# Optimization experiments

Hardware: AMD Instinct MI355X
Metric: run time of the kernel (lower is better)

The kernel has to match this reference:

```python
import jax, jax.numpy as jnp
import numpy as np

N = 16384       # nodes (hits in one event)
IN_DIM = 9      # input features per hit
HID = 128       # hidden_dim
PROP = 64       # propagate_dimensions; 2*PROP == HID so all gravnet layers share shapes
SPACE = 4       # learned space dimensions
K = 40          # neighbors (includes self, matching torch_cluster.knn)
L = 4           # num_gravnet_layers
OUT_DIM = 4


def _lin(key, fan_in, fan_out):
    # torch nn.Linear default init: U(-1/sqrt(fan_in), 1/sqrt(fan_in))
    k1, k2 = jax.random.split(key)
    lim = 1.0 / np.sqrt(fan_in)
    W = jax.random.uniform(k1, (fan_in, fan_out), minval=-lim, maxval=lim, dtype=jnp.float32)
    b = jax.random.uniform(k2, (fan_out,), minval=-lim, maxval=lim, dtype=jnp.float32)
    return W, b


def _stack_lin(key, fan_in, fan_out, n):
    Ws, bs = [], []
    for i in range(n):
        W, b = _lin(jax.random.fold_in(key, i), fan_in, fan_out)
        Ws.append(W); bs.append(b)
    return jnp.stack(Ws), jnp.stack(bs)


def setup_inputs() -> dict:
    key = jax.random.key(0)
    ks = jax.random.split(key, 16)
    inp = {}
    inp['x'] = jax.random.normal(ks[0], (N, IN_DIM), dtype=jnp.float32)
    inp['fc1_W'], inp['fc1_b'] = _lin(ks[1], IN_DIM, HID)
    inp['fc2_W'], inp['fc2_b'] = _lin(ks[2], HID, HID)
    # GravNetConv params (in_channels = HID = 2*PROP for every layer)
    inp['gs_W'], inp['gs_b'] = _stack_lin(ks[3], HID, SPACE, L)          # lin_s
    inp['gh_W'], inp['gh_b'] = _stack_lin(ks[4], HID, PROP, L)           # lin_h
    inp['go_W'], inp['go_b'] = _stack_lin(ks[5], HID + 2 * PROP, 2 * PROP, L)  # lin_out
    # dense_after_gravnet: Linear(2P->HID), Linear(HID->HID), Linear(HID->2P)
    inp['d1_W'], inp['d1_b'] = _stack_lin(ks[6], 2 * PROP, HID, L)
    inp['d2_W'], inp['d2_b'] = _stack_lin(ks[7], HID, HID, L)
    inp['d3_W'], inp['d3_b'] = _stack_lin(ks[8], HID, 2 * PROP, L)
    inp['fc3_W'], inp['fc3_b'] = _lin(ks[9], 2 * PROP, HID)
    inp['fc4_W'], inp['fc4_b'] = _lin(ks[10], HID, OUT_DIM)
    return inp


def _gravnet_layer(x, sW, sb, hW, hb, oW, ob):
    # PyG GravNetConv: s = lin_s(x), h = lin_h(x); kNN in s-space (self included);
    # edge weight exp(-10*d^2); message h_j*w; aggr = [mean, max]; out = lin_out([x, aggr]).
    s = x @ sW + sb                               # [N, SPACE]
    h = x @ hW + hb                               # [N, PROP]
    s2 = jnp.sum(s * s, axis=1)
    d2 = s2[:, None] + s2[None, :] - 2.0 * (s @ s.T)   # [N, N] squared distances
    neg_d2, idx = jax.lax.top_k(-d2, K)           # k nearest (self is its own nearest)
    w = jnp.exp(10.0 * jnp.minimum(neg_d2, 0.0))  # exp(-10*d2), clamped d2 >= 0
    msg = h[idx] * w[..., None]                   # [N, K, PROP] gather + weight
    agg = jnp.concatenate([msg.mean(axis=1), msg.max(axis=1)], axis=-1)  # [N, 2P]
    return jnp.concatenate([x, agg], axis=-1) @ oW + ob


def reference(x, fc1_W, fc1_b, fc2_W, fc2_b, gs_W, gs_b, gh_W, gh_b, go_W, go_b,
              d1_W, d1_b, d2_W, d2_b, d3_W, d3_b, fc3_W, fc3_b, fc4_W, fc4_b):
    relu = jax.nn.relu
    x = relu(x @ fc1_W + fc1_b)
    x = relu(x @ fc2_W + fc2_b)
    for i in range(L):  # small fixed layer count
        x = _gravnet_layer(x, gs_W[i], gs_b[i], gh_W[i], gh_b[i], go_W[i], go_b[i])
        x = relu(x @ d1_W[i] + d1_b[i])
        x = relu(x @ d2_W[i] + d2_b[i])
        x = relu(x @ d3_W[i] + d3_b[i])
    x = relu(x @ fc3_W + fc3_b)
    return x @ fc4_W + fc4_b
```

## Files before the change

kernel.cpp:

```cpp
#include <hip/hip_runtime.h>
#include <math.h>

#define NPTS     16384
#define KNN_K    40
#define KNN_CAPW 320

typedef unsigned short u16;
typedef __attribute__((ext_vector_type(8))) short bf16x8;
typedef __attribute__((ext_vector_type(4))) float f32x4;

static __device__ __forceinline__ float bf2f(unsigned short h) {
  return __uint_as_float(((unsigned)h) << 16);
}
static __device__ __forceinline__ unsigned short f2bf(float f) {
  unsigned u = __float_as_uint(f);
  unsigned r = (u + 0x7fffu + ((u >> 16) & 1u)) >> 16;
  return (unsigned short)r;
}
static __device__ __forceinline__ float ldf(const float* p) { return *p; }
static __device__ __forceinline__ float ldf(const unsigned short* p) { return bf2f(*p); }

static __device__ __forceinline__ float rfl(float x) {
  return __uint_as_float(__builtin_amdgcn_readfirstlane(__float_as_uint(x)));
}
static __device__ __forceinline__ unsigned mbcnt64(unsigned long long m) {
  return __builtin_amdgcn_mbcnt_hi((unsigned)(m >> 32),
                                   __builtin_amdgcn_mbcnt_lo((unsigned)m, 0u));
}

static __device__ __forceinline__ unsigned encf(float f) {
  unsigned b = __float_as_uint(f);
  return (b & 0x80000000u) ? ~b : (b | 0x80000000u);
}
static __device__ __forceinline__ float decf(unsigned e) {
  unsigned b = (e & 0x80000000u) ? (e ^ 0x80000000u) : ~e;
  return __uint_as_float(b);
}

#define WSPLIT_ELEMS 393216

__global__ __launch_bounds__(256, 8) void wsplit_k(
    const float* __restrict__ fc2W, const float* __restrict__ ghW,
    const float* __restrict__ goW,  const float* __restrict__ d1W,
    const float* __restrict__ d2W,  const float* __restrict__ d3W,
    const float* __restrict__ fc3W, u16* __restrict__ out)
{
  int e = blockIdx.x * 256 + threadIdx.x;
  const float* W; int base, lM;
  if (e < 16384)       { W = fc2W; base = 0;      lM = 7; }
  else if (e < 49152)  { W = ghW;  base = 16384;  lM = 6; }
  else if (e < 180224) { W = goW;  base = 49152;  lM = 7; }
  else if (e < 245760) { W = d1W;  base = 180224; lM = 7; }
  else if (e < 311296) { W = d2W;  base = 245760; lM = 7; }
  else if (e < 376832) { W = d3W;  base = 311296; lM = 7; }
  else                 { W = fc3W; base = 376832; lM = 7; }
  int li = e - base;
  int M = 1 << lM;
  int k = li >> lM, n = li & (M - 1);
  float wv = W[li];
  u16 hi = f2bf(wv);
  u16 lo = f2bf(wv - bf2f(hi));
  int kb = k >> 5, kk = k & 31;
  u16* ob = out + 2 * base + kb * (M << 6);
  ob[n * 32 + kk] = hi;
  ob[(M << 5) + n * 32 + kk] = lo;
}

template<int MCOLS, bool RELU>
__global__ __launch_bounds__(256, 2) void gemm_mfma_k(
    const u16* __restrict__ A1, int lda1,
    const u16* __restrict__ A2, int lda2, int K1,
    const u16* __restrict__ Wsp, const float* __restrict__ bias,
    u16* __restrict__ C, int ldc, int K)
{
  constexpr int CT = MCOLS / 64;
  constexpr int AST = 40;
  __shared__ u16 lds[64 * AST + 2 * MCOLS * AST];
  u16* As = lds;
  u16* Wh = lds + 64 * AST;
  u16* Wl = Wh + MCOLS * AST;

  const int tid = threadIdx.x;
  const int lane = tid & 63;
  const int w = tid >> 6;
  const int row0 = blockIdx.x * 64;

  f32x4 acc[4][CT];
  #pragma unroll
  for (int rt = 0; rt < 4; ++rt)
    #pragma unroll
    for (int ct = 0; ct < CT; ++ct)
      acc[rt][ct] = (f32x4){0.f, 0.f, 0.f, 0.f};

  const int rbase = lane & 15;
  const int koff = (lane >> 4) * 8;

  for (int k0 = 0, kb = 0; k0 < K; k0 += 32, ++kb) {
    __syncthreads();
    {
      int r = tid >> 2, seg = tid & 3;
      int kk = k0 + seg * 8;
      const u16* src = (kk < K1) ? &A1[(size_t)(row0 + r) * lda1 + kk]
                                 : &A2[(size_t)(row0 + r) * lda2 + (kk - K1)];
      *(uint4*)&As[r * AST + seg * 8] = *(const uint4*)src;
    }
    {
      const u16* wsb = Wsp + (size_t)kb * (MCOLS << 6);
      #pragma unroll
      for (int l = tid; l < 2 * MCOLS * 4; l += 256) {
        int r = l >> 2, seg = l & 3;
        *(uint4*)&Wh[r * AST + seg * 8] = *(const uint4*)&wsb[r * 32 + seg * 8];
      }
    }
    __syncthreads();

    bf16x8 a[4];
    #pragma unroll
    for (int rt = 0; rt < 4; ++rt)
      a[rt] = *(const bf16x8*)&As[(rt * 16 + rbase) * AST + koff];
    #pragma unroll
    for (int ct = 0; ct < CT; ++ct) {
      int col = (w * CT + ct) * 16 + rbase;
      bf16x8 bh = *(const bf16x8*)&Wh[col * AST + koff];
      bf16x8 bl = *(const bf16x8*)&Wl[col * AST + koff];
      #pragma unroll
      for (int rt = 0; rt < 4; ++rt) {
        acc[rt][ct] = __builtin_amdgcn_mfma_f32_16x16x32_bf16(a[rt], bh, acc[rt][ct], 0, 0, 0);
        acc[rt][ct] = __builtin_amdgcn_mfma_f32_16x16x32_bf16(a[rt], bl, acc[rt][ct], 0, 0, 0);
      }
    }
  }

  __syncthreads();
  constexpr int CST = MCOLS + 8;
  u16* Ct = lds;
  const int rq = (lane >> 4) * 4;
  #pragma unroll
  for (int ct = 0; ct < CT; ++ct) {
    int col = (w * CT + ct) * 16 + rbase;
    float bv = bias[col];
    #pragma unroll
    for (int rt = 0; rt < 4; ++rt) {
      #pragma unroll
      for (int q = 0; q < 4; ++q) {
        float v = acc[rt][ct][q] + bv;
        if (RELU) v = fmaxf(v, 0.f);
        Ct[(rt * 16 + rq + q) * CST + col] = f2bf(v);
      }
    }
  }
  __syncthreads();
  constexpr int SEGS = MCOLS / 8;
  for (int l = tid; l < 64 * SEGS; l += 256) {
    int r = l / SEGS, sg = l % SEGS;
    *(uint4*)&C[(size_t)(row0 + r) * ldc + sg * 8] = *(const uint4*)&Ct[r * CST + sg * 8];
  }
}

template<int MCOLS, bool RELU>
__global__ __launch_bounds__(256, 2) void gemm_mfma_f32_k(
    const u16* __restrict__ A1, int lda1,
    const u16* __restrict__ A2, int lda2, int K1,
    const float* __restrict__ W, const float* __restrict__ bias,
    u16* __restrict__ C, int ldc, int K)
{
  constexpr int CT = MCOLS / 64;
  constexpr int AST = 40;
  __shared__ u16 lds[64 * AST + 2 * MCOLS * AST];
  u16* As = lds;
  u16* Wh = lds + 64 * AST;
  u16* Wl = Wh + MCOLS * AST;

  const int tid = threadIdx.x;
  const int lane = tid & 63;
  const int w = tid >> 6;
  const int row0 = blockIdx.x * 64;

  f32x4 acc[4][CT];
  #pragma unroll
  for (int rt = 0; rt < 4; ++rt)
    #pragma unroll
    for (int ct = 0; ct < CT; ++ct)
      acc[rt][ct] = (f32x4){0.f, 0.f, 0.f, 0.f};

  const int rbase = lane & 15;
  const int koff = (lane >> 4) * 8;

  for (int k0 = 0; k0 < K; k0 += 32) {
    __syncthreads();
    {
      int r = tid >> 2, seg = tid & 3;
      int kk = k0 + seg * 8;
      const u16* src = (kk < K1) ? &A1[(size_t)(row0 + r) * lda1 + kk]
                                 : &A2[(size_t)(row0 + r) * lda2 + (kk - K1)];
      *(uint4*)&As[r * AST + seg * 8] = *(const uint4*)src;
    }
    for (int l = tid; l < 32 * MCOLS; l += 256) {
      int n = l & (MCOLS - 1), kk = l / MCOLS;
      float wv = W[(size_t)(k0 + kk) * MCOLS + n];
      u16 h = f2bf(wv);
      Wh[n * AST + kk] = h;
      Wl[n * AST + kk] = f2bf(wv - bf2f(h));
    }
    __syncthreads();

    bf16x8 a[4];
    #pragma unroll
    for (int rt = 0; rt < 4; ++rt)
      a[rt] = *(const bf16x8*)&As[(rt * 16 + rbase) * AST + koff];
    #pragma unroll
    for (int ct = 0; ct < CT; ++ct) {
      int col = (w * CT + ct) * 16 + rbase;
      bf16x8 bh = *(const bf16x8*)&Wh[col * AST + koff];
      bf16x8 bl = *(const bf16x8*)&Wl[col * AST + koff];
      #pragma unroll
      for (int rt = 0; rt < 4; ++rt) {
        acc[rt][ct] = __builtin_amdgcn_mfma_f32_16x16x32_bf16(a[rt], bh, acc[rt][ct], 0, 0, 0);
        acc[rt][ct] = __builtin_amdgcn_mfma_f32_16x16x32_bf16(a[rt], bl, acc[rt][ct], 0, 0, 0);
      }
    }
  }

  __syncthreads();
  constexpr int CST = MCOLS + 8;
  u16* Ct = lds;
  const int rq = (lane >> 4) * 4;
  #pragma unroll
  for (int ct = 0; ct < CT; ++ct) {
    int col = (w * CT + ct) * 16 + rbase;
    float bv = bias[col];
    #pragma unroll
    for (int rt = 0; rt < 4; ++rt) {
      #pragma unroll
      for (int q = 0; q < 4; ++q) {
        float v = acc[rt][ct][q] + bv;
        if (RELU) v = fmaxf(v, 0.f);
        Ct[(rt * 16 + rq + q) * CST + col] = f2bf(v);
      }
    }
  }
  __syncthreads();
  constexpr int SEGS = MCOLS / 8;
  for (int l = tid; l < 64 * SEGS; l += 256) {
    int r = l / SEGS, sg = l % SEGS;
    *(uint4*)&C[(size_t)(row0 + r) * ldc + sg * 8] = *(const uint4*)&Ct[r * CST + sg * 8];
  }
}

template<int MCOLS, bool RELU, typename TIN, typename TOUT>
__global__ __launch_bounds__(256, 4) void gemm_k(
    const TIN* __restrict__ A1, int lda1,
    const TIN* __restrict__ A2, int lda2, int K1,
    const float* __restrict__ W, const float* __restrict__ bias,
    TOUT* __restrict__ C, int ldc, int K)
{
  constexpr int TCS = MCOLS / 8;
  constexpr int RPT = (64 * TCS) / 256;
  __shared__ float Asl[64][33];
  __shared__ float Ws[32][MCOLS];
  const int tid = threadIdx.x;
  const int row0 = blockIdx.x * 64;
  const int tc = tid % TCS, tr = tid / TCS;

  float acc[RPT][8];
  #pragma unroll
  for (int p = 0; p < RPT; ++p)
    #pragma unroll
    for (int q = 0; q < 8; ++q) acc[p][q] = 0.f;

  for (int k0 = 0; k0 < K; k0 += 32) {
    __syncthreads();
    for (int l = tid; l < 64 * 32; l += 256) {
      int r = l >> 5, c = l & 31, k = k0 + c;
      float v = 0.f;
      if (k < K) v = (k < K1) ? ldf(&A1[(size_t)(row0 + r) * lda1 + k])
                              : ldf(&A2[(size_t)(row0 + r) * lda2 + (k - K1)]);
      Asl[r][c] = v;
    }
    for (int l = tid; l < 32 * MCOLS; l += 256) {
      int kr = l / MCOLS, c = l % MCOLS, k = k0 + kr;
      Ws[kr][c] = (k < K) ? W[(size_t)k * MCOLS + c] : 0.f;
    }
    __syncthreads();
    #pragma unroll
    for (int kk = 0; kk < 32; ++kk) {
      float a[RPT];
      #pragma unroll
      for (int p = 0; p < RPT; ++p) a[p] = Asl[tr * RPT + p][kk];
      const float4 w0 = *(const float4*)&Ws[kk][tc * 8];
      const float4 w1 = *(const float4*)&Ws[kk][tc * 8 + 4];
      #pragma unroll
      for (int p = 0; p < RPT; ++p) {
        acc[p][0] = fmaf(a[p], w0.x, acc[p][0]);
        acc[p][1] = fmaf(a[p], w0.y, acc[p][1]);
        acc[p][2] = fmaf(a[p], w0.z, acc[p][2]);
        acc[p][3] = fmaf(a[p], w0.w, acc[p][3]);
        acc[p][4] = fmaf(a[p], w1.x, acc[p][4]);
        acc[p][5] = fmaf(a[p], w1.y, acc[p][5]);
        acc[p][6] = fmaf(a[p], w1.z, acc[p][6]);
        acc[p][7] = fmaf(a[p], w1.w, acc[p][7]);
      }
    }
  }

  const float4 b0 = *(const float4*)&bias[tc * 8];
  const float4 b1 = *(const float4*)&bias[tc * 8 + 4];
  #pragma unroll
  for (int p = 0; p < RPT; ++p) {
    int r = row0 + tr * RPT + p;
    float o[8];
    o[0] = acc[p][0] + b0.x; o[1] = acc[p][1] + b0.y;
    o[2] = acc[p][2] + b0.z; o[3] = acc[p][3] + b0.w;
    o[4] = acc[p][4] + b1.x; o[5] = acc[p][5] + b1.y;
    o[6] = acc[p][6] + b1.z; o[7] = acc[p][7] + b1.w;
    if (RELU) {
      #pragma unroll
      for (int q = 0; q < 8; ++q) o[q] = fmaxf(o[q], 0.f);
    }
    if constexpr (sizeof(TOUT) == 2) {
      unsigned p0 = (unsigned)f2bf(o[0]) | ((unsigned)f2bf(o[1]) << 16);
      unsigned p1 = (unsigned)f2bf(o[2]) | ((unsigned)f2bf(o[3]) << 16);
      unsigned p2 = (unsigned)f2bf(o[4]) | ((unsigned)f2bf(o[5]) << 16);
      unsigned p3 = (unsigned)f2bf(o[6]) | ((unsigned)f2bf(o[7]) << 16);
      uint4 pk = make_uint4(p0, p1, p2, p3);
      *(uint4*)&C[(size_t)r * ldc + tc * 8] = pk;
    } else {
      float4 o0, o1;
      o0.x = o[0]; o0.y = o[1]; o0.z = o[2]; o0.w = o[3];
      o1.x = o[4]; o1.y = o[5]; o1.z = o[6]; o1.w = o[7];
      *(float4*)&C[(size_t)r * ldc + tc * 8] = o0;
      *(float4*)&C[(size_t)r * ldc + tc * 8 + 4] = o1;
    }
  }
}

template<bool RELU, bool MM, typename TOUT>
__global__ __launch_bounds__(256, 4) void gemm4_k(
    const u16* __restrict__ A, int lda,
    const float* __restrict__ W, const float* __restrict__ bias,
    TOUT* __restrict__ C, int K, unsigned* mm)
{
  __shared__ float Wsl[128 * 4];
  __shared__ float bl[4];
  const int tid = threadIdx.x;
  for (int l = tid; l < K * 4; l += 256) Wsl[l] = W[l];
  if (tid < 4) bl[tid] = bias[tid];
  __syncthreads();
  const int row = blockIdx.x * 256 + tid;
  const u16* ap = A + (size_t)row * lda;
  float a0 = bl[0], a1 = bl[1], a2 = bl[2], a3 = bl[3];
  for (int k8 = 0; k8 < K; k8 += 8) {
    uint4 pk = *(const uint4*)&ap[k8];
    unsigned uu[4] = {pk.x, pk.y, pk.z, pk.w};
    #pragma unroll
    for (int q = 0; q < 4; ++q) {
      float flo = __uint_as_float(uu[q] << 16);
      float fhi = __uint_as_float(uu[q] & 0xFFFF0000u);
      const float* wr0 = &Wsl[(k8 + 2 * q) * 4];
      a0 = fmaf(flo, wr0[0], a0); a1 = fmaf(flo, wr0[1], a1);
      a2 = fmaf(flo, wr0[2], a2); a3 = fmaf(flo, wr0[3], a3);
      a0 = fmaf(fhi, wr0[4], a0); a1 = fmaf(fhi, wr0[5], a1);
      a2 = fmaf(fhi, wr0[6], a2); a3 = fmaf(fhi, wr0[7], a3);
    }
  }
  if (RELU) {
    a0 = fmaxf(a0, 0.f); a1 = fmaxf(a1, 0.f);
    a2 = fmaxf(a2, 0.f); a3 = fmaxf(a3, 0.f);
  }
  if constexpr (sizeof(TOUT) == 2) {
    C[(size_t)row * 4 + 0] = (TOUT)f2bf(a0);
    C[(size_t)row * 4 + 1] = (TOUT)f2bf(a1);
    C[(size_t)row * 4 + 2] = (TOUT)f2bf(a2);
    C[(size_t)row * 4 + 3] = (TOUT)f2bf(a3);
  } else {
    float4 o; o.x = a0; o.y = a1; o.z = a2; o.w = a3;
    *(float4*)&C[(size_t)row * 4] = o;
  }
  if constexpr (MM) {
    float mn0 = a0, mx0 = a0, mn1 = a1, mx1 = a1;
    float mn2 = a2, mx2 = a2, mn3 = a3, mx3 = a3;
    #pragma unroll
    for (int o = 32; o >= 1; o >>= 1) {
      mn0 = fminf(mn0, __shfl_xor(mn0, o, 64)); mx0 = fmaxf(mx0, __shfl_xor(mx0, o, 64));
      mn1 = fminf(mn1, __shfl_xor(mn1, o, 64)); mx1 = fmaxf(mx1, __shfl_xor(mx1, o, 64));
      mn2 = fminf(mn2, __shfl_xor(mn2, o, 64)); mx2 = fmaxf(mx2, __shfl_xor(mx2, o, 64));
      mn3 = fminf(mn3, __shfl_xor(mn3, o, 64)); mx3 = fmaxf(mx3, __shfl_xor(mx3, o, 64));
    }
    if ((tid & 63) == 0) {
      atomicMin(&mm[0], encf(mn0)); atomicMax(&mm[4], encf(mx0));
      atomicMin(&mm[1], encf(mn1)); atomicMax(&mm[5], encf(mx1));
      atomicMin(&mm[2], encf(mn2)); atomicMax(&mm[6], encf(mx2));
      atomicMin(&mm[3], encf(mn3)); atomicMax(&mm[7], encf(mx3));
    }
  }
}

__global__ void init_mm_k(unsigned* mm) {
  int t = threadIdx.x;
  if (t < 4) { mm[t] = 0xFFFFFFFFu; mm[4 + t] = 0u; }
}

static __device__ __forceinline__ float dimsel(float4 p, int d) {
  return (d == 0) ? p.x : (d == 1) ? p.y : (d == 2) ? p.z : p.w;
}

__global__ __launch_bounds__(1024, 1) void histpref_k(
    const float* __restrict__ S, unsigned* __restrict__ mm,
    unsigned* __restrict__ binoff)
{
  __shared__ unsigned hist[256];
  __shared__ unsigned wsum[4];
  const int tid = threadIdx.x;
  float mn[4], rg[4];
  #pragma unroll
  for (int d = 0; d < 4; ++d) {
    mn[d] = decf(mm[d]);
    rg[d] = decf(mm[4 + d]) - mn[d];
  }
  int a = 0;
  #pragma unroll
  for (int d = 1; d < 4; ++d) if (rg[d] > rg[a]) a = d;
  int b = (a == 0) ? 1 : 0;
  #pragma unroll
  for (int d = 0; d < 4; ++d) if (d != a && rg[d] > rg[b]) b = d;
  float inva = (rg[a] > 0.f) ? (16.f / rg[a]) * 0.999999f : 0.f;
  float invb = (rg[b] > 0.f) ? (16.f / rg[b]) * 0.999999f : 0.f;
  if (tid == 0) {
    mm[8] = (unsigned)a; mm[9] = (unsigned)b;
    mm[10] = __float_as_uint(mn[a]); mm[11] = __float_as_uint(inva);
    mm[12] = __float_as_uint(mn[b]); mm[13] = __float_as_uint(invb);
  }
  if (tid < 256) hist[tid] = 0u;
  __syncthreads();
  for (int i = tid; i < NPTS; i += 1024) {
    float4 p = *(const float4*)&S[(size_t)i * 4];
    int ba = min(15, max(0, (int)((dimsel(p, a) - mn[a]) * inva)));
    int bb = min(15, max(0, (int)((dimsel(p, b) - mn[b]) * invb)));
    atomicAdd(&hist[ba * 16 + bb], 1u);
  }
  __syncthreads();
  unsigned v = 0, x = 0;
  if (tid < 256) {
    int lane = tid & 63;
    v = hist[tid]; x = v;
    #pragma unroll
    for (int o = 1; o < 64; o <<= 1) {
      unsigned t = (unsigned)__shfl_up((int)x, o, 64);
      if (lane >= o) x += t;
    }
    if (lane == 63) wsum[tid >> 6] = x;
  }
  __syncthreads();
  if (tid < 256) {
    unsigned off = 0;
    for (int k = 0; k < (tid >> 6); ++k) off += wsum[k];
    binoff[tid] = off + x - v;
  }
}

__global__ __launch_bounds__(256, 4) void scatter_k(
    const float* __restrict__ S, const unsigned* __restrict__ mm,
    unsigned* __restrict__ binoff,
    float4* __restrict__ SX4, float* __restrict__ SS2, u16* __restrict__ SIDXs)
{
  int a = (int)mm[8], b = (int)mm[9];
  float alo = __uint_as_float(mm[10]), inva = __uint_as_float(mm[11]);
  float blo = __uint_as_float(mm[12]), invb = __uint_as_float(mm[13]);
  int i = blockIdx.x * 256 + threadIdx.x;
  float4 p = *(const float4*)&S[(size_t)i * 4];
  int ba = min(15, max(0, (int)((dimsel(p, a) - alo) * inva)));
  int bb = min(15, max(0, (int)((dimsel(p, b) - blo) * invb)));
  unsigned pos = atomicAdd(&binoff[ba * 16 + bb], 1u);
  SX4[pos] = p;
  SS2[pos] = fmaf(p.x, p.x, fmaf(p.y, p.y, fmaf(p.z, p.z, p.w * p.w)));
  SIDXs[pos] = (u16)i;
}

__global__ __launch_bounds__(512, 4) void gaabb_k(const float4* __restrict__ SX4,
                                                  float* __restrict__ gaabb) {
  int w = threadIdx.x >> 6, lane = threadIdx.x & 63;
  int g = blockIdx.x * 8 + w;
  float4 p = SX4[g * 64 + lane];
  float mnx = p.x, mny = p.y, mnz = p.z, mnw = p.w;
  float mxx = p.x, mxy = p.y, mxz = p.z, mxw = p.w;
  #pragma unroll
  for (int o = 32; o >= 1; o >>= 1) {
    mnx = fminf(mnx, __shfl_xor(mnx, o, 64)); mxx = fmaxf(mxx, __shfl_xor(mxx, o, 64));
    mny = fminf(mny, __shfl_xor(mny, o, 64)); mxy = fmaxf(mxy, __shfl_xor(mxy, o, 64));
    mnz = fminf(mnz, __shfl_xor(mnz, o, 64)); mxz = fmaxf(mxz, __shfl_xor(mxz, o, 64));
    mnw = fminf(mnw, __shfl_xor(mnw, o, 64)); mxw = fmaxf(mxw, __shfl_xor(mxw, o, 64));
  }
  if (lane == 0) {
    float4* gp = (float4*)&gaabb[g * 8];
    gp[0] = make_float4(mnx, mny, mnz, mnw);
    gp[1] = make_float4(mxx, mxy, mxz, mxw);
  }
}

struct CompactRes { int cnt; unsigned thr; };

static __device__ __forceinline__ CompactRes compact_buf(unsigned* bufR, int cnt, int lane) {
  int n = min(cnt, KNN_CAPW);
  int lo = -1, hi = 0x7FFFFFFF, chi = n;
  for (int it = 0; it < 32; ++it) {
    if (chi <= 96) break;
    int mid = lo + ((hi - lo) >> 1);
    int lc = 0;
    for (int base = 0; base < n; base += 64) {
      int i = base + lane;
      bool c = (i < n) && (bufR[i] <= (unsigned)mid);
      lc += (int)__popcll(__ballot(c));
    }
    if (lc >= 40) { hi = mid; chi = lc; } else lo = mid;
  }
  unsigned thr = (unsigned)hi;
  int out = 0;
  for (int base = 0; base < n; base += 64) {
    int i = base + lane;
    unsigned key = (i < n) ? bufR[i] : 0xFFFFFFFFu;
    bool keep = (i < n) && (key <= thr);
    unsigned long long mk = __ballot(keep);
    unsigned pre = mbcnt64(mk);
    if (keep) bufR[out + (int)pre] = key;
    out += (int)__popcll(mk);
  }
  CompactRes r; r.cnt = out; r.thr = thr;
  return r;
}

__global__ __launch_bounds__(256, 4) void knn_k(
    const float4* __restrict__ SX4, const float* __restrict__ SS2,
    const u16* __restrict__ SIDXs, const float* __restrict__ gaabb,
    u16* __restrict__ idx_out, u16* __restrict__ w_out)
{
  __shared__ unsigned buf[4 * 4 * KNN_CAPW];
  __shared__ unsigned scr[4 * 128];
  __shared__ int cnts[16];
  __shared__ unsigned thrend[16];
  __shared__ unsigned short glist[4 * 64];
  __shared__ unsigned long long mws[4];
  __shared__ unsigned thrsh[4];

  const int tid = threadIdx.x;
  const int lane = tid & 63;
  const int w = tid >> 6;
  const int sp0 = blockIdx.x * 4;

  float cx[4], cy[4], cz[4], cw[4], s2r[4], thrF[4];
  int orow[4], cnt[4];
  #pragma unroll
  for (int r = 0; r < 4; ++r) {
    float4 sr = SX4[sp0 + r];
    cx[r] = rfl(-2.f * sr.x); cy[r] = rfl(-2.f * sr.y);
    cz[r] = rfl(-2.f * sr.z); cw[r] = rfl(-2.f * sr.w);
    s2r[r] = rfl(fmaf(sr.x, sr.x, fmaf(sr.y, sr.y, fmaf(sr.z, sr.z, sr.w * sr.w))));
    orow[r] = SIDXs[sp0 + r];
    cnt[r] = 0;
  }
  unsigned* bufw = &buf[w * 4 * KNN_CAPW];
  unsigned* mph = buf;

  {
    int gs = sp0 >> 6;
    int g0 = min(max(gs - 7, 0), 240);
    float m1[4], m2[4];
    #pragma unroll
    for (int r = 0; r < 4; ++r) { m1[r] = 3.0e38f; m2[r] = 3.0e38f; }
    #pragma unroll
    for (int gi = 0; gi < 4; ++gi) {
      int j = (g0 + w * 4 + gi) * 64 + lane;
      float4 p = SX4[j];
      float q = SS2[j];
      #pragma unroll
      for (int r = 0; r < 4; ++r) {
        float d = fmaf(cx[r], p.x, fmaf(cy[r], p.y, fmaf(cz[r], p.z,
                  fmaf(cw[r], p.w, q + s2r[r]))));
        d = fmaxf(d, 0.f);
        bool lt1 = d < m1[r];
        float nm2 = lt1 ? m1[r] : fminf(m2[r], d);
        m1[r] = fminf(m1[r], d);
        m2[r] = nm2;
      }
    }
    #pragma unroll
    for (int r = 0; r < 4; ++r) {
      mph[(r * 8 + w * 2 + 0) * 64 + lane] = __float_as_uint(m1[r]);
      mph[(r * 8 + w * 2 + 1) * 64 + lane] = __float_as_uint(m2[r]);
    }
  }
  __syncthreads();

  {
    unsigned vals[8];
    #pragma unroll
    for (int s = 0; s < 8; ++s) vals[s] = mph[(w * 8 + s) * 64 + lane];
    int lo = -1, hi = 0x7F800000, chi = 512;
    for (int it = 0; it < 32; ++it) {
      if (chi <= 44 || (hi - lo) <= 1) break;
      int mid = lo + ((hi - lo) >> 1);
      int c = 0;
      #pragma unroll
      for (int s = 0; s < 8; ++s)
        c += (int)__popcll(__ballot(vals[s] <= (unsigned)mid));
      if (c >= 40) { hi = mid; chi = c; } else lo = mid;
    }
    if (lane == 0) thrsh[w] = (unsigned)hi;
  }
  __syncthreads();
  #pragma unroll
  for (int r = 0; r < 4; ++r) thrF[r] = __uint_as_float(thrsh[r]);

  {
    int g = w * 64 + lane;
    float4 mn = *(const float4*)&gaabb[g * 8];
    float4 mx = *(const float4*)&gaabb[g * 8 + 4];
    bool want = false;
    #pragma unroll
    for (int r = 0; r < 4; ++r) {
      float px = -0.5f * cx[r], py = -0.5f * cy[r];
      float pz = -0.5f * cz[r], pw = -0.5f * cw[r];
      float dx = fmaxf(fmaxf(mn.x - px, px - mx.x), 0.f);
      float dy = fmaxf(fmaxf(mn.y - py, py - mx.y), 0.f);
      float dz = fmaxf(fmaxf(mn.z - pz, pz - mx.z), 0.f);
      float dw = fmaxf(fmaxf(mn.w - pw, pw - mx.w), 0.f);
      float md = fmaf(dx, dx, fmaf(dy, dy, fmaf(dz, dz, dw * dw)));
      want |= (md <= thrF[r]);
    }
    unsigned long long bal = __ballot(want);
    if (lane == 0) mws[w] = bal;
  }
  __syncthreads();

  int ng = 0;
  {
    int ordbase = 0;
    #pragma unroll
    for (int pgi = 0; pgi < 4; ++pgi) {
      unsigned long long m = mws[pgi];
      bool want = (m >> lane) & 1ull;
      int ord = ordbase + (int)mbcnt64(m);
      if (want && ((ord & 3) == w))
        glist[w * 64 + (ord >> 2)] = (unsigned short)(pgi * 64 + lane);
      ordbase += (int)__popcll(m);
    }
    ng = (ordbase + 3 - w) >> 2;
  }

  if (ng > 0) {
    int j = (int)glist[w * 64] * 64 + lane;
    float4 p = SX4[j];
    float q = SS2[j];
    unsigned sv = (unsigned)j;
    for (int i = 0; i < ng; ++i) {
      float4 pn = p; float qn = q; unsigned svn = sv;
      if (i + 1 < ng) {
        int j2 = (int)glist[w * 64 + i + 1] * 64 + lane;
        pn = SX4[j2]; qn = SS2[j2]; svn = (unsigned)j2;
      }
      #pragma unroll
      for (int r = 0; r < 4; ++r) {
        float d = fmaf(cx[r], p.x, fmaf(cy[r], p.y, fmaf(cz[r], p.z,
                  fmaf(cw[r], p.w, q + s2r[r]))));
        bool k = d <= thrF[r];
        unsigned long long mk = __ballot(k);
        if (mk) {
          int pos = cnt[r] + (int)mbcnt64(mk);
          if (k) bufw[r * KNN_CAPW + pos] =
              (__float_as_uint(fmaxf(d, 0.f)) & 0xFFFFC000u) | sv;
          cnt[r] += (int)__popcll(mk);
          if (cnt[r] >= KNN_CAPW - 64) {
            CompactRes cr = compact_buf(&bufw[r * KNN_CAPW], cnt[r], lane);
            cnt[r] = cr.cnt;
            thrF[r] = __uint_as_float((cr.thr & 0xFFFFC000u) | 0x3FFFu);
          }
        }
      }
      p = pn; q = qn; sv = svn;
    }
  }

  if (lane == 0) {
    #pragma unroll
    for (int r = 0; r < 4; ++r) {
      cnts[w * 4 + r] = cnt[r];
      thrend[w * 4 + r] = (__float_as_uint(thrF[r]) & 0xFFFFC000u) | 0x3FFFu;
    }
  }
  __syncthreads();

  {
    const int rr = w;
    const unsigned* seg[4];
    int c[4], off[5];
    off[0] = 0;
    #pragma unroll
    for (int s = 0; s < 4; ++s) {
      seg[s] = &buf[(s * 4 + rr) * KNN_CAPW];
      c[s] = cnts[s * 4 + rr];
      off[s + 1] = off[s] + c[s];
    }
    int mt = off[4];
    unsigned* S = &scr[rr * 128];

    if (mt > 128) {
      unsigned hi0 = min(min(thrend[0 * 4 + rr], thrend[1 * 4 + rr]),
                         min(thrend[2 * 4 + rr], thrend[3 * 4 + rr]));
      int lc = 0;
      #pragma unroll
      for (int s = 0; s < 4; ++s)
        for (int base = 0; base < c[s]; base += 64) {
          int i = base + lane;
          bool cc = (i < c[s]) && (seg[s][i] <= hi0);
          lc += (int)__popcll(__ballot(cc));
        }
      unsigned thrm = hi0;
      if (lc > 128) {
        int lo = -1, hi = (int)hi0, chi = lc;
        for (int it = 0; it < 32; ++it) {
          if (chi <= 96) break;
          int mid = lo + ((hi - lo) >> 1);
          int lc2 = 0;
          #pragma unroll
          for (int s = 0; s < 4; ++s)
            for (int base = 0; base < c[s]; base += 64) {
              int i = base + lane;
              bool cc = (i < c[s]) && (seg[s][i] <= (unsigned)mid);
              lc2 += (int)__popcll(__ballot(cc));
            }
          if (lc2 >= 40) { hi = mid; chi = lc2; } else lo = mid;
        }
        thrm = (unsigned)hi;
      }
      int out = 0;
      #pragma unroll
      for (int s = 0; s < 4; ++s)
        for (int base = 0; base < c[s]; base += 64) {
          int i = base + lane;
          unsigned key = (i < c[s]) ? seg[s][i] : 0xFFFFFFFFu;
          bool keep = (i < c[s]) && (key <= thrm);
          unsigned long long mk = __ballot(keep);
          int pos = out + (int)mbcnt64(mk);
          if (keep && pos < 128) S[pos] = key;
          out += (int)__popcll(mk);
        }
      mt = min(out, 128);
    } else {
      #pragma unroll
      for (int s = 0; s < 4; ++s)
        for (int base = 0; base < c[s]; base += 64) {
          int i = base + lane;
          if (i < c[s]) S[off[s] + i] = seg[s][i];
        }
    }

    const float fx = cx[rr], fy = cy[rr], fz = cz[rr], fw = cw[rr];
    const float s2i = s2r[rr];
    const int row = orow[rr];

    unsigned long long e0 = ~0ull, e1 = ~0ull;
    {
      int sl0 = lane * 2, sl1 = lane * 2 + 1;
      if (sl0 < mt) {
        unsigned key = S[sl0];
        unsigned sj = key & 0x3FFFu;
        float4 p = SX4[sj];
        float qj = fmaf(p.x, p.x, fmaf(p.y, p.y, fmaf(p.z, p.z, p.w * p.w)));
        float d = fmaf(fx, p.x, fmaf(fy, p.y, fmaf(fz, p.z, fmaf(fw, p.w, qj + s2i))));
        unsigned oi = (unsigned)SIDXs[sj];
        e0 = (((unsigned long long)__float_as_uint(fmaxf(d, 0.f))) << 32) | oi;
      }
      if (sl1 < mt) {
        unsigned key = S[sl1];
        unsigned sj = key & 0x3FFFu;
        float4 p = SX4[sj];
        float qj = fmaf(p.x, p.x, fmaf(p.y, p.y, fmaf(p.z, p.z, p.w * p.w)));
        float d = fmaf(fx, p.x, fmaf(fy, p.y, fmaf(fz, p.z, fmaf(fw, p.w, qj + s2i))));
        unsigned oi = (unsigned)SIDXs[sj];
        e1 = (((unsigned long long)__float_as_uint(fmaxf(d, 0.f))) << 32) | oi;
      }
    }

    #pragma unroll
    for (int k = 2; k <= 128; k <<= 1) {
      #pragma unroll
      for (int jj = k >> 1; jj >= 1; jj >>= 1) {
        bool up = (((lane * 2) & k) == 0);
        if (jj == 1) {
          unsigned long long a = (e0 < e1) ? e0 : e1;
          unsigned long long b = (e0 < e1) ? e1 : e0;
          e0 = up ? a : b; e1 = up ? b : a;
        } else {
          int lj = jj >> 1;
          bool lower = ((lane & lj) == 0);
          bool tm = (up == lower);
          unsigned long long o0 = __shfl_xor(e0, lj, 64);
          e0 = tm ? ((e0 < o0) ? e0 : o0) : ((e0 > o0) ? e0 : o0);
          unsigned long long o1 = __shfl_xor(e1, lj, 64);
          e1 = tm ? ((e1 < o1) ? e1 : o1) : ((e1 > o1) ? e1 : o1);
        }
      }
    }

    const int ob = row * KNN_K;
    if (lane < 20) {
      int v0 = lane * 2;
      idx_out[ob + v0] = (unsigned short)(e0 & 0xFFFFu);
      w_out[ob + v0] = f2bf(__expf(-10.f * __uint_as_float((unsigned)(e0 >> 32))));
      int v1 = v0 + 1;
      idx_out[ob + v1] = (unsigned short)(e1 & 0xFFFFu);
      w_out[ob + v1] = f2bf(__expf(-10.f * __uint_as_float((unsigned)(e1 >> 32))));
    }
  }
}

__global__ __launch_bounds__(256, 4) void agg_k(
    const unsigned short* __restrict__ h, const unsigned short* __restrict__ idxb,
    const unsigned short* __restrict__ wb, unsigned short* __restrict__ Aout)
{
  const int row = blockIdx.x * 4 + (threadIdx.x >> 6);
  const int lane = threadIdx.x & 63;
  const int base = row * KNN_K;
  float mean = 0.f, mx = -INFINITY;
  #pragma unroll 4
  for (int k = 0; k < KNN_K; ++k) {
    int j = idxb[base + k];
    float wv = bf2f(wb[base + k]);
    float m = bf2f(h[(size_t)j * 64 + lane]) * wv;
    mean += m;
    mx = fmaxf(mx, m);
  }
  Aout[(size_t)row * 128 + lane] = f2bf(mean * (1.f / 40.f));
  Aout[(size_t)row * 128 + 64 + lane] = f2bf(mx);
}

extern "C" void kernel_launch(void* const* d_in, const int* in_sizes, int n_in,
                              void* d_out, int out_size, void* d_ws, size_t ws_size,
                              hipStream_t stream)
{
  const float* x    = (const float*)d_in[0];
  const float* fc1W = (const float*)d_in[1];  const float* fc1b = (const float*)d_in[2];
  const float* fc2W = (const float*)d_in[3];  const float* fc2b = (const float*)d_in[4];
  const float* gsW  = (const float*)d_in[5];  const float* gsb  = (const float*)d_in[6];
  const float* ghW  = (const float*)d_in[7];  const float* ghb  = (const float*)d_in[8];
  const float* goW  = (const float*)d_in[9];  const float* gob  = (const float*)d_in[10];
  const float* d1W  = (const float*)d_in[11]; const float* d1b  = (const float*)d_in[12];
  const float* d2W  = (const float*)d_in[13]; const float* d2b  = (const float*)d_in[14];
  const float* d3W  = (const float*)d_in[15]; const float* d3b  = (const float*)d_in[16];
  const float* fc3W = (const float*)d_in[17]; const float* fc3b = (const float*)d_in[18];
  const float* fc4W = (const float*)d_in[19]; const float* fc4b = (const float*)d_in[20];
  float* out = (float*)d_out;

  const size_t N = NPTS;
  u16* X    = (u16*)d_ws;
  u16* Abuf = X + N * 128;
  u16* T    = Abuf + N * 128;
  u16* IDX  = T + N * 128;
  u16* WNB  = IDX + N * 40;
  float4* SX4g = (float4*)(WNB + N * 40);
  float*  SS2g = (float*)(SX4g + N);
  u16*    SIDXg = (u16*)(SS2g + N);
  unsigned* binoff = (unsigned*)(SIDXg + N);
  unsigned* mm     = binoff + 256;
  float* gaabbg    = (float*)(mm + 16);
  float* S = (float*)Abuf;
  u16* H = T;

  u16* WSPL = (u16*)(gaabbg + 256 * 8);
  size_t needed = (size_t)((char*)(WSPL + 2ull * WSPLIT_ELEMS) - (char*)d_ws);
  const bool PRE = ws_size >= needed;

  const size_t OF_FC2 = 0,      OF_GH = 32768, OF_GO = 98304;
  const size_t OF_D1 = 360448,  OF_D2 = 491520, OF_D3 = 622592, OF_FC3 = 753664;
  const size_t ST_GH = 16384, ST_GO = 65536, ST_D = 32768;

  if (PRE) {
    wsplit_k<<<WSPLIT_ELEMS / 256, 256, 0, stream>>>(
        fc2W, ghW, goW, d1W, d2W, d3W, fc3W, WSPL);
  }

  gemm_k<128, true, float, u16><<<NPTS / 64, 256, 0, stream>>>(
      x, 9, x, 9, 9, fc1W, fc1b, T, 128, 9);
  if (PRE)
    gemm_mfma_k<128, true><<<NPTS / 64, 256, 0, stream>>>(
        T, 128, T, 128, 128, WSPL + OF_FC2, fc2b, X, 128, 128);
  else
    gemm_mfma_f32_k<128, true><<<NPTS / 64, 256, 0, stream>>>(
        T, 128, T, 128, 128, fc2W, fc2b, X, 128, 128);

  for (int l = 0; l < 4; ++l) {
    init_mm_k<<<1, 64, 0, stream>>>(mm);
    gemm4_k<false, true, float><<<NPTS / 256, 256, 0, stream>>>(
        X, 128, gsW + l * 128 * 4, gsb + l * 4, S, 128, mm);
    if (PRE)
      gemm_mfma_k<64, false><<<NPTS / 64, 256, 0, stream>>>(
          X, 128, X, 128, 128, WSPL + OF_GH + l * ST_GH, ghb + l * 64, H, 64, 128);
    else
      gemm_mfma_f32_k<64, false><<<NPTS / 64, 256, 0, stream>>>(
          X, 128, X, 128, 128, ghW + l * 128 * 64, ghb + l * 64, H, 64, 128);
    histpref_k<<<1, 1024, 0, stream>>>(S, mm, binoff);
    scatter_k<<<NPTS / 256, 256, 0, stream>>>(S, mm, binoff, SX4g, SS2g, SIDXg);
    gaabb_k<<<32, 512, 0, stream>>>(SX4g, gaabbg);
    knn_k<<<NPTS / 4, 256, 0, stream>>>(SX4g, SS2g, SIDXg, gaabbg, IDX, WNB);
    agg_k<<<NPTS / 4, 256, 0, stream>>>(H, IDX, WNB, Abuf);
    if (PRE) {
      gemm_mfma_k<128, false><<<NPTS / 64, 256, 0, stream>>>(
          X, 128, Abuf, 128, 128, WSPL + OF_GO + l * ST_GO, gob + l * 128, T, 128, 256);
      gemm_mfma_k<128, true><<<NPTS / 64, 256, 0, stream>>>(
          T, 128, T, 128, 128, WSPL + OF_D1 + l * ST_D, d1b + l * 128, Abuf, 128, 128);
      gemm_mfma_k<128, true><<<NPTS / 64, 256, 0, stream>>>(
          Abuf, 128, Abuf, 128, 128, WSPL + OF_D2 + l * ST_D, d2b + l * 128, T, 128, 128);
      gemm_mfma_k<128, true><<<NPTS / 64, 256, 0, stream>>>(
          T, 128, T, 128, 128, WSPL + OF_D3 + l * ST_D, d3b + l * 128, X, 128, 128);
    } else {
      gemm_mfma_f32_k<128, false><<<NPTS / 64, 256, 0, stream>>>(
          X, 128, Abuf, 128, 128, goW + l * 256 * 128, gob + l * 128, T, 128, 256);
      gemm_mfma_f32_k<128, true><<<NPTS / 64, 256, 0, stream>>>(
          T, 128, T, 128, 128, d1W + l * 128 * 128, d1b + l * 128, Abuf, 128, 128);
      gemm_mfma_f32_k<128, true><<<NPTS / 64, 256, 0, stream>>>(
          Abuf, 128, Abuf, 128, 128, d2W + l * 128 * 128, d2b + l * 128, T, 128, 128);
      gemm_mfma_f32_k<128, true><<<NPTS / 64, 256, 0, stream>>>(
          T, 128, T, 128, 128, d3W + l * 128 * 128, d3b + l * 128, X, 128, 128);
    }
  }

  if (PRE)
    gemm_mfma_k<128, true><<<NPTS / 64, 256, 0, stream>>>(
        X, 128, X, 128, 128, WSPL + OF_FC3, fc3b, T, 128, 128);
  else
    gemm_mfma_f32_k<128, true><<<NPTS / 64, 256, 0, stream>>>(
        X, 128, X, 128, 128, fc3W, fc3b, T, 128, 128);
  gemm4_k<false, false, float><<<NPTS / 256, 256, 0, stream>>>(
      T, 128, fc4W, fc4b, out, 128, mm);
}
```

Measured before the change: 1.080 ms.

## Split MFMA GEMMs into 64-column panels and use bitonic sort for kNN threshold

The split-bf16 GEMM kernel now computes one 64-column output panel per block, and 128-column outputs launch twice as many blocks. The weight pre-split kernel is reordered into a per-layer, per-panel layout so each block reads one contiguous panel. This raises the block count, which should help occupancy on a wide GPU, at the cost of loading the A tile twice. Separately, the kNN threshold search replaces an iterative binary search over ballots with a wave-wide bitonic sort of per-lane top-2 minima and takes the 40th smallest value.

```diff
diff --git a/kernel.cpp b/kernel.cpp
--- a/kernel.cpp
+++ b/kernel.cpp
@@ -46,34 +46,37 @@
     const float* __restrict__ fc3W, u16* __restrict__ out)
 {
   int e = blockIdx.x * 256 + threadIdx.x;
-  const float* W; int base, lM;
-  if (e < 16384)       { W = fc2W; base = 0;      lM = 7; }
-  else if (e < 49152)  { W = ghW;  base = 16384;  lM = 6; }
-  else if (e < 180224) { W = goW;  base = 49152;  lM = 7; }
-  else if (e < 245760) { W = d1W;  base = 180224; lM = 7; }
-  else if (e < 311296) { W = d2W;  base = 245760; lM = 7; }
-  else if (e < 376832) { W = d3W;  base = 311296; lM = 7; }
-  else                 { W = fc3W; base = 376832; lM = 7; }
+  const float* W; int base, M, K;
+  if (e < 16384)       { W = fc2W; base = 0;      M = 128; K = 128; }
+  else if (e < 49152)  { W = ghW;  base = 16384;  M = 64;  K = 128; }
+  else if (e < 180224) { W = goW;  base = 49152;  M = 128; K = 256; }
+  else if (e < 245760) { W = d1W;  base = 180224; M = 128; K = 128; }
+  else if (e < 311296) { W = d2W;  base = 245760; M = 128; K = 128; }
+  else if (e < 376832) { W = d3W;  base = 311296; M = 128; K = 128; }
+  else                 { W = fc3W; base = 376832; M = 128; K = 128; }
   int li = e - base;
-  int M = 1 << lM;
-  int k = li >> lM, n = li & (M - 1);
   float wv = W[li];
   u16 hi = f2bf(wv);
   u16 lo = f2bf(wv - bf2f(hi));
-  int kb = k >> 5, kk = k & 31;
-  u16* ob = out + 2 * base + kb * (M << 6);
-  ob[n * 32 + kk] = hi;
-  ob[(M << 5) + n * 32 + kk] = lo;
-}
-
-template<int MCOLS, bool RELU>
+  int row = li / M;
+  int n   = li % M;
+  int l   = row / K;
+  int kl  = row % K;
+  int p   = n >> 6, c = n & 63;
+  int kb  = kl >> 5, kk = kl & 31;
+  u16* ob = out + 2 * base + l * (2 * K * M) + p * (K * 128) + kb * 4096;
+  ob[c * 32 + kk] = hi;
+  ob[2048 + c * 32 + kk] = lo;
+}
+
+template<bool RELU>
 __global__ __launch_bounds__(256, 2) void gemm_mfma_k(
     const u16* __restrict__ A1, int lda1,
     const u16* __restrict__ A2, int lda2, int K1,
-    const u16* __restrict__ Wsp, const float* __restrict__ bias,
+    const u16* __restrict__ Wsp, int pstride, const float* __restrict__ bias,
     u16* __restrict__ C, int ldc, int K)
 {
-  constexpr int CT = MCOLS / 64;
+  constexpr int MCOLS = 64;
   constexpr int AST = 40;
   __shared__ u16 lds[64 * AST + 2 * MCOLS * AST];
   u16* As = lds;
@@ -83,14 +86,16 @@
   const int tid = threadIdx.x;
   const int lane = tid & 63;
   const int w = tid >> 6;
-  const int row0 = blockIdx.x * 64;
-
-  f32x4 acc[4][CT];
+  const int panel = blockIdx.x >> 8;
+  const int row0 = (blockIdx.x & 255) * 64;
+  Wsp += (size_t)panel * pstride;
+  bias += panel * 64;
+  C += panel * 64;
+
+  f32x4 acc[4];
   #pragma unroll
   for (int rt = 0; rt < 4; ++rt)
-    #pragma unroll
-    for (int ct = 0; ct < CT; ++ct)
-      acc[rt][ct] = (f32x4){0.f, 0.f, 0.f, 0.f};
+    acc[rt] = (f32x4){0.f, 0.f, 0.f, 0.f};
 
   const int rbase = lane & 15;
   const int koff = (lane >> 4) * 8;
@@ -105,7 +110,7 @@
       *(uint4*)&As[r * AST + seg * 8] = *(const uint4*)src;
     }
     {
-      const u16* wsb = Wsp + (size_t)kb * (MCOLS << 6);
+      const u16* wsb = Wsp + (size_t)kb * 4096;
       #pragma unroll
       for (int l = tid; l < 2 * MCOLS * 4; l += 256) {
         int r = l >> 2, seg = l & 3;
@@ -118,15 +123,14 @@
     #pragma unroll
     for (int rt = 0; rt < 4; ++rt)
       a[rt] = *(const bf16x8*)&As[(rt * 16 + rbase) * AST + koff];
-    #pragma unroll
-    for (int ct = 0; ct < CT; ++ct) {
-      int col = (w * CT + ct) * 16 + rbase;
+    {
+      int col = w * 16 + rbase;
       bf16x8 bh = *(const bf16x8*)&Wh[col * AST + koff];
       bf16x8 bl = *(const bf16x8*)&Wl[col * AST + koff];
       #pragma unroll
       for (int rt = 0; rt < 4; ++rt) {
-        acc[rt][ct] = __builtin_amdgcn_mfma_f32_16x16x32_bf16(a[rt], bh, acc[rt][ct], 0, 0, 0);
-        acc[rt][ct] = __builtin_amdgcn_mfma_f32_16x16x32_bf16(a[rt], bl, acc[rt][ct], 0, 0, 0);
+        acc[rt] = __builtin_amdgcn_mfma_f32_16x16x32_bf16(a[rt], bh, acc[rt], 0, 0, 0);
+        acc[rt] = __builtin_amdgcn_mfma_f32_16x16x32_bf16(a[rt], bl, acc[rt], 0, 0, 0);
       }
     }
   }
@@ -135,15 +139,14 @@
   constexpr int CST = MCOLS + 8;
   u16* Ct = lds;
   const int rq = (lane >> 4) * 4;
-  #pragma unroll
-  for (int ct = 0; ct < CT; ++ct) {
-    int col = (w * CT + ct) * 16 + rbase;
+  {
+    int col = w * 16 + rbase;
     float bv = bias[col];
     #pragma unroll
     for (int rt = 0; rt < 4; ++rt) {
       #pragma unroll
       for (int q = 0; q < 4; ++q) {
-        float v = acc[rt][ct][q] + bv;
+        float v = acc[rt][q] + bv;
         if (RELU) v = fmaxf(v, 0.f);
         Ct[(rt * 16 + rq + q) * CST + col] = f2bf(v);
       }
@@ -591,20 +594,37 @@
   __syncthreads();
 
   {
-    unsigned vals[8];
-    #pragma unroll
-    for (int s = 0; s < 8; ++s) vals[s] = mph[(w * 8 + s) * 64 + lane];
-    int lo = -1, hi = 0x7F800000, chi = 512;
-    for (int it = 0; it < 32; ++it) {
-      if (chi <= 44 || (hi - lo) <= 1) break;
-      int mid = lo + ((hi - lo) >> 1);
-      int c = 0;
-      #pragma unroll
-      for (int s = 0; s < 8; ++s)
-        c += (int)__popcll(__ballot(vals[s] <= (unsigned)mid));
-      if (c >= 40) { hi = mid; chi = c; } else lo = mid;
-    }
-    if (lane == 0) thrsh[w] = (unsigned)hi;
+    unsigned m1 = 0xFFFFFFFFu, m2 = 0xFFFFFFFFu;
+    #pragma unroll
+    for (int s = 0; s < 8; ++s) {
+      unsigned v = mph[(w * 8 + s) * 64 + lane];
+      bool lt = v < m1;
+      unsigned nm2 = lt ? m1 : min(m2, v);
+      m1 = min(m1, v);
+      m2 = nm2;
+    }
+    unsigned e0 = m1, e1 = m2;
+    #pragma unroll
+    for (int k = 2; k <= 128; k <<= 1) {
+      #pragma unroll
+      for (int jj = k >> 1; jj >= 1; jj >>= 1) {
+        bool up = (((lane * 2) & k) == 0);
+        if (jj == 1) {
+          unsigned a = min(e0, e1), b = max(e0, e1);
+          e0 = up ? a : b; e1 = up ? b : a;
+        } else {
+          int lj = jj >> 1;
+          bool lower = ((lane & lj) == 0);
+          bool tm = (up == lower);
+          unsigned o0 = (unsigned)__shfl_xor((int)e0, lj, 64);
+          e0 = tm ? min(e0, o0) : max(e0, o0);
+          unsigned o1 = (unsigned)__shfl_xor((int)e1, lj, 64);
+          e1 = tm ? min(e1, o1) : max(e1, o1);
+        }
+      }
+    }
+    unsigned v40 = (unsigned)__shfl((int)e1, 19, 64);
+    if (lane == 0) thrsh[w] = v40;
   }
   __syncthreads();
   #pragma unroll
@@ -871,7 +891,9 @@
 
   const size_t OF_FC2 = 0,      OF_GH = 32768, OF_GO = 98304;
   const size_t OF_D1 = 360448,  OF_D2 = 491520, OF_D3 = 622592, OF_FC3 = 753664;
-  const size_t ST_GH = 16384, ST_GO = 65536, ST_D = 32768;
+  const int PS_128 = 16384;
+  const int PS_256 = 32768;
+  const size_t LS_GH = 16384, LS_GO = 65536, LS_D = 32768;
 
   if (PRE) {
     wsplit_k<<<WSPLIT_ELEMS / 256, 256, 0, stream>>>(
@@ -881,8 +903,8 @@
   gemm_k<128, true, float, u16><<<NPTS / 64, 256, 0, stream>>>(
       x, 9, x, 9, 9, fc1W, fc1b, T, 128, 9);
   if (PRE)
-    gemm_mfma_k<128, true><<<NPTS / 64, 256, 0, stream>>>(
-        T, 128, T, 128, 128, WSPL + OF_FC2, fc2b, X, 128, 128);
+    gemm_mfma_k<true><<<512, 256, 0, stream>>>(
+        T, 128, T, 128, 128, WSPL + OF_FC2, PS_128, fc2b, X, 128, 128);
   else
     gemm_mfma_f32_k<128, true><<<NPTS / 64, 256, 0, stream>>>(
         T, 128, T, 128, 128, fc2W, fc2b, X, 128, 128);
@@ -892,8 +914,8 @@
     gemm4_k<false, true, float><<<NPTS / 256, 256, 0, stream>>>(
         X, 128, gsW + l * 128 * 4, gsb + l * 4, S, 128, mm);
     if (PRE)
-      gemm_mfma_k<64, false><<<NPTS / 64, 256, 0, stream>>>(
-          X, 128, X, 128, 128, WSPL + OF_GH + l * ST_GH, ghb + l * 64, H, 64, 128);
+      gemm_mfma_k<false><<<256, 256, 0, stream>>>(
+          X, 128, X, 128, 128, WSPL + OF_GH + l * LS_GH, PS_128, ghb + l * 64, H, 64, 128);
     else
       gemm_mfma_f32_k<64, false><<<NPTS / 64, 256, 0, stream>>>(
           X, 128, X, 128, 128, ghW + l * 128 * 64, ghb + l * 64, H, 64, 128);
@@ -903,14 +925,14 @@
     knn_k<<<NPTS / 4, 256, 0, stream>>>(SX4g, SS2g, SIDXg, gaabbg, IDX, WNB);
     agg_k<<<NPTS / 4, 256, 0, stream>>>(H, IDX, WNB, Abuf);
     if (PRE) {
-      gemm_mfma_k<128, false><<<NPTS / 64, 256, 0, stream>>>(
-          X, 128, Abuf, 128, 128, WSPL + OF_GO + l * ST_GO, gob + l * 128, T, 128, 256);
-      gemm_mfma_k<128, true><<<NPTS / 64, 256, 0, stream>>>(
-          T, 128, T, 128, 128, WSPL + OF_D1 + l * ST_D, d1b + l * 128, Abuf, 128, 128);
-      gemm_mfma_k<128, true><<<NPTS / 64, 256, 0, stream>>>(
-          Abuf, 128, Abuf, 128, 128, WSPL + OF_D2 + l * ST_D, d2b + l * 128, T, 128, 128);
-      gemm_mfma_k<128, true><<<NPTS / 64, 256, 0, stream>>>(
-          T, 128, T, 128, 128, WSPL + OF_D3 + l * ST_D, d3b + l * 128, X, 128, 128);
+      gemm_mfma_k<false><<<512, 256, 0, stream>>>(
+          X, 128, Abuf, 128, 128, WSPL + OF_GO + l * LS_GO, PS_256, gob + l * 128, T, 128, 256);
+      gemm_mfma_k<true><<<512, 256, 0, stream>>>(
+          T, 128, T, 128, 128, WSPL + OF_D1 + l * LS_D, PS_128, d1b + l * 128, Abuf, 128, 128);
+      gemm_mfma_k<true><<<512, 256, 0, stream>>>(
+          Abuf, 128, Abuf, 128, 128, WSPL + OF_D2 + l * LS_D, PS_128, d2b + l * 128, T, 128, 128);
+      gemm_mfma_k<true><<<512, 256, 0, stream>>>(
+          T, 128, T, 128, 128, WSPL + OF_D3 + l * LS_D, PS_128, d3b + l * 128, X, 128, 128);
     } else {
       gemm_mfma_f32_k<128, false><<<NPTS / 64, 256, 0, stream>>>(
           X, 128, Abuf, 128, 128, goW + l * 256 * 128, gob + l * 128, T, 128, 256);
@@ -924,8 +946,8 @@
   }
 
   if (PRE)
-    gemm_mfma_k<128, true><<<NPTS / 64, 256, 0, stream>>>(
-        X, 128, X, 128, 128, WSPL + OF_FC3, fc3b, T, 128, 128);
+    gemm_mfma_k<true><<<512, 256, 0, stream>>>(
+        X, 128, X, 128, 128, WSPL + OF_FC3, PS_128, fc3b, T, 128, 128);
   else
     gemm_mfma_f32_k<128, true><<<NPTS / 64, 256, 0, stream>>>(
         X, 128, X, 128, 128, fc3W, fc3b, T, 128, 128);
```

New measurement: 1.016 ms. 5.9% less time.
